# Performance work log

Hardware: AMD Instinct MI355X
Metric: run time of the kernel (lower is better)

The kernel has to match this reference:

```python
import jax, jax.numpy as jnp
import numpy as np

B, T, H, N, D, L, V = 4, 1024, 4, 4096, 256, 6, 256
Dh = N // H  # per-head dim; RoPE max_pos == Dh so T <= Dh
EPS = 1e-5


def _ln(x):
    # LayerNorm over last dim, no affine, eps=1e-5 (torch default)
    m = jnp.mean(x, axis=-1, keepdims=True)
    v = jnp.mean((x - m) ** 2, axis=-1, keepdims=True)
    return (x - m) / jnp.sqrt(v + EPS)


def _rope_tables(seq_len, head_dim):
    inv_freq = 1.0 / (10000.0 ** (jnp.arange(0, head_dim, 2, dtype=jnp.float32) / head_dim))
    t = jnp.arange(seq_len, dtype=jnp.float32)
    freqs = jnp.outer(t, inv_freq)            # [T, Dh/2]
    emb = jnp.concatenate([freqs, freqs], -1)  # [T, Dh]
    return jnp.cos(emb), jnp.sin(emb)


def _rotate_half(x):
    d = x.shape[-1]
    return jnp.concatenate([-x[..., d // 2:], x[..., :d // 2]], axis=-1)


def setup_inputs() -> dict:
    key = jax.random.key(0)
    ks = jax.random.split(key, 6)
    tokens = jax.random.randint(ks[0], (B, T), 0, V)
    emb_w = 0.02 * jax.random.normal(ks[1], (V, D), dtype=jnp.float32)
    E = 0.02 * jax.random.normal(ks[2], (N, D), dtype=jnp.float32)
    Dx = 0.02 * jax.random.normal(ks[3], (H, D, Dh), dtype=jnp.float32)
    Dy = 0.02 * jax.random.normal(ks[4], (H, D, Dh), dtype=jnp.float32)
    readout = 0.02 * jax.random.normal(ks[5], (D, V), dtype=jnp.float32)
    return {"tokens": tokens, "emb_w": emb_w, "E": E, "Dx": Dx, "Dy": Dy, "readout": readout}


def reference(tokens, emb_w, E, Dx, Dy, readout):
    b, t = tokens.shape
    dh = Dx.shape[-1]
    cos, sin = _rope_tables(t, dh)  # [T, Dh], broadcast over B,H
    v = _ln(emb_w[tokens])          # [B, T, D]
    for _ in range(L):
        x = jax.nn.relu(jnp.einsum('btd,hde->bhte', v, Dx))       # [B,H,T,Dh]
        xr = x * cos + _rotate_half(x) * sin                       # RoPE (Q and K share)
        scores = jnp.einsum('bhte,bhse->bhts', xr, xr)             # [B,H,T,T] (no softmax)
        a = jnp.einsum('bhts,bsd->bhtd', scores, v)                # [B,H,T,D]
        y = jax.nn.relu(jnp.einsum('bhtd,hde->bhte', a, Dy)) * x   # [B,H,T,Dh]
        y = jnp.transpose(y, (0, 2, 1, 3)).reshape(b, t, -1)       # [B,T,N]
        v = _ln(v + _ln(y @ E))
    return v @ readout  # [B,T,V]
```

## Files before the change

### kernel.cpp

```cpp
#include <hip/hip_runtime.h>
#include <cstdint>

namespace {

typedef _Float16 f16_t;
typedef _Float16 f16x8 __attribute__((ext_vector_type(8)));
typedef _Float16 f16x4 __attribute__((ext_vector_type(4)));
typedef float    f32x4 __attribute__((ext_vector_type(4)));
typedef float    f32x16 __attribute__((ext_vector_type(16)));

constexpr int Bc = 4, Tc = 1024, Hc = 4, Dc = 256, DHc = 1024, Lc = 6, Vc = 256;
constexpr int HALFc = 512;
constexpr float EPS = 1e-5f;
constexpr long long T4q  = (long long)Tc * 4096;
constexpr long long TDq  = (long long)Tc * Dc;
constexpr long long HDDq = (long long)DHc * Dc;
constexpr long long TBUFq = (long long)Bc * Tc * Dc;

__device__ __forceinline__ int pe_perm(int v) {
  return (v & ~1023) | ((v & 511) << 1) | ((v >> 9) & 1);
}

__device__ __forceinline__ void gload16(const void* g, void* l) {
  __builtin_amdgcn_global_load_lds((const __attribute__((address_space(1))) void*)g,
                                   (__attribute__((address_space(3))) void*)l, 16, 0, 0);
}


template<int NW>
__device__ __forceinline__ void stage_kmaj(const f16_t* __restrict__ P, int k0,
                                           int ld, int c0, f16_t* S, int tid) {
  if constexpr (NW == 16) {
    const int cg = tid & 15;
    const int kp = (tid >> 4) & 31;
    const int jh = (tid >> 9) * 4;
    const int k  = kp * 2;
    const f16x4 r0 = *(const f16x4*)(P + (size_t)(k0 + k) * ld + c0 + cg * 8 + jh);
    const f16x4 r1 = *(const f16x4*)(P + (size_t)(k0 + k + 1) * ld + c0 + cg * 8 + jh);
    #pragma unroll
    for (int j = 0; j < 4; ++j) {
      const int n = cg * 8 + jh + j;
      union { f16_t h[2]; unsigned int u; } pk;
      pk.h[0] = r0[j]; pk.h[1] = r1[j];
      ((unsigned int*)S)[n * 32 + ((((kp >> 2) ^ (n & 7) ^ ((n >> 3) & 7)) & 7) << 2)
                         + (kp & 3)] = pk.u;
    }
  } else {
    const int cg  = tid & 15;
    const int kpb = tid >> 4;
    constexpr int NP = (NW == 4) ? 2 : 1;
    #pragma unroll
    for (int p = 0; p < NP; ++p) {
      const int kp = p * 16 + kpb;
      const int k  = kp * 2;
      const f16x8 r0 = *(const f16x8*)(P + (size_t)(k0 + k) * ld + c0 + cg * 8);
      const f16x8 r1 = *(const f16x8*)(P + (size_t)(k0 + k + 1) * ld + c0 + cg * 8);
      #pragma unroll
      for (int j = 0; j < 8; ++j) {
        const int n = cg * 8 + j;
        union { f16_t h[2]; unsigned int u; } pk;
        pk.h[0] = r0[j]; pk.h[1] = r1[j];
        ((unsigned int*)S)[n * 32 + ((((kp >> 2) ^ (n & 7) ^ ((n >> 3) & 7)) & 7) << 2)
                           + (kp & 3)] = pk.u;
      }
    }
  }
}

template<int EPI, bool AKMAJ, bool BKMAJ, int NW, int KU, bool GRPZ>
__global__ __launch_bounds__(NW * 64)
void gemm_f16(const f16_t* __restrict__ A, long long sAb, long long sAh,
              const f16_t* __restrict__ B, long long sBb, long long sBh,
              void* __restrict__ Cv, long long sCb, long long sCh,
              const f16_t* __restrict__ aux,
              int K, int lda, int ldb, int ldc,
              const float* __restrict__ cosP, const float* __restrict__ sinP)
{
  constexpr int FN2  = (NW == 4) ? 2 : 1;
  constexpr int MT   = (NW == 16) ? 1 : 2;
  constexpr int WCW  = FN2 * 32;
  constexpr int WRH  = MT * 32;
  constexpr int NTHR = NW * 64;
  constexpr int SP   = 1024 / NTHR;
  constexpr int RPP  = NTHR / 8;

  __shared__ __align__(16) f16_t As[KU][128 * 64];
  __shared__ __align__(16) f16_t Bs[KU][128 * 64];

  int bx = blockIdx.x, by = blockIdx.y, bz = blockIdx.z;
  if (GRPZ) {
    const int Xd = gridDim.x, Zd = gridDim.z;
    const int f  = blockIdx.x + Xd * (blockIdx.y + gridDim.y * blockIdx.z);
    bz = f % Zd;
    const int rem = f / Zd;
    bx = rem % Xd;
    by = rem / Xd;
  }

  const int zb = bz >> 2, zh = bz & 3;
  A += zb * sAb + zh * sAh;
  B += zb * sBb + zh * sBh;
  const long long Coff = zb * sCb + zh * sCh;

  const int tid  = threadIdx.x;
  const int lane = tid & 63;
  const int wave = tid >> 6;
  const int wr = (NW == 4) ? (wave >> 1) : (wave >> 2);
  const int wc = (NW == 4) ? (wave & 1)  : (wave & 3);
  const int m0 = by * 128, n0 = bx * 128;

  const int lrow  = tid >> 3;
  const int lslot = tid & 7;

  f32x16 acc[MT][FN2] = {};

  for (int k0 = 0; k0 < K; k0 += KU * 64) {
    #pragma unroll
    for (int u = 0; u < KU; ++u) {
      const int ku = k0 + u * 64;
      if (!AKMAJ) {
        #pragma unroll
        for (int c = 0; c < SP; ++c) {
          const int row  = c * RPP + lrow;
          const int scol = ((lslot ^ (row & 7) ^ ((row >> 3) & 7)) << 3);
          gload16(A + (size_t)(m0 + row) * lda + ku + scol, &As[u][(c * NTHR + tid) * 8]);
        }
      } else {
        stage_kmaj<NW>(A, ku, lda, m0, As[u], tid);
      }
      if (!BKMAJ) {
        #pragma unroll
        for (int c = 0; c < SP; ++c) {
          const int row  = c * RPP + lrow;
          const int scol = ((lslot ^ (row & 7) ^ ((row >> 3) & 7)) << 3);
          gload16(B + (size_t)(n0 + row) * ldb + ku + scol, &Bs[u][(c * NTHR + tid) * 8]);
        }
      } else {
        stage_kmaj<NW>(B, ku, ldb, n0, Bs[u], tid);
      }
    }
    __syncthreads();

    #pragma unroll
    for (int u = 0; u < KU; ++u) {
      #pragma unroll
      for (int kc = 0; kc < 4; ++kc) {
        f16x8 af[MT], bf[FN2];
        #pragma unroll
        for (int m = 0; m < MT; ++m) {
          const int r  = wr * WRH + m * 32 + (lane & 31);
          const int sl = (kc * 2 + (lane >> 5)) ^ (r & 7) ^ ((r >> 3) & 7);
          af[m] = *(const f16x8*)(&As[u][r * 64 + sl * 8]);
        }
        #pragma unroll
        for (int n = 0; n < FN2; ++n) {
          const int r  = wc * WCW + n * 32 + (lane & 31);
          const int sl = (kc * 2 + (lane >> 5)) ^ (r & 7) ^ ((r >> 3) & 7);
          bf[n] = *(const f16x8*)(&Bs[u][r * 64 + sl * 8]);
        }
        #pragma unroll
        for (int m = 0; m < MT; ++m)
          #pragma unroll
          for (int n = 0; n < FN2; ++n)
            acc[m][n] = __builtin_amdgcn_mfma_f32_32x32x16_f16(af[m], bf[n], acc[m][n], 0, 0, 0);
      }
    }
    __syncthreads();
  }

  const int rbase = 4 * (lane >> 5);
  if (EPI == 4) {
    float* C = (float*)Cv + Coff;
    #pragma unroll
    for (int m = 0; m < MT; ++m)
      #pragma unroll
      for (int n = 0; n < FN2; ++n) {
        const int gcol = n0 + wc * WCW + n * 32 + (lane & 31);
        #pragma unroll
        for (int reg = 0; reg < 16; ++reg) {
          const int grow = m0 + wr * WRH + m * 32 + (reg & 3) + 8 * (reg >> 2) + rbase;
          C[(long long)grow * ldc + gcol] = acc[m][n][reg];
        }
      }
  } else if (EPI == 5) {
    f16_t* C = (f16_t*)Cv + Coff;
    #pragma unroll
    for (int m = 0; m < MT; ++m)
      #pragma unroll
      for (int n = 0; n < FN2; ++n) {
        const int gcol = n0 + wc * WCW + n * 32 + (lane & 31);
        const int jj   = (gcol & 1023) >> 1;
        const float sg = (gcol & 1) ? 1.0f : -1.0f;
        #pragma unroll
        for (int reg = 0; reg < 16; ++reg) {
          const int grow = m0 + wr * WRH + m * 32 + (reg & 3) + 8 * (reg >> 2) + rbase;
          const int tt   = grow & (Tc - 1);
          const float val  = fmaxf(acc[m][n][reg], 0.0f);
          const float part = __shfl_xor(val, 1);
          const float c = cosP[tt * HALFc + jj];
          const float s = sinP[tt * HALFc + jj];
          C[(long long)grow * ldc + gcol] = (f16_t)(val * c + part * s * sg);
        }
      }
  } else if (EPI == 2) {
    f16_t* C = (f16_t*)Cv + Coff;
    const f16_t* X = aux + Coff;
    #pragma unroll
    for (int m = 0; m < MT; ++m)
      #pragma unroll
      for (int n = 0; n < FN2; ++n) {
        const int gcol = n0 + wc * WCW + n * 32 + (lane & 31);
        const int jj   = (gcol & 1023) >> 1;
        const float sg = (gcol & 1) ? 1.0f : -1.0f;
        #pragma unroll
        for (int reg = 0; reg < 16; ++reg) {
          const int grow = m0 + wr * WRH + m * 32 + (reg & 3) + 8 * (reg >> 2) + rbase;
          const int tt   = grow & (Tc - 1);
          const long long off = (long long)grow * ldc + gcol;
          const float xrv  = (float)X[off];
          const float part = __shfl_xor(xrv, 1);
          const float c = cosP[tt * HALFc + jj];
          const float s = sinP[tt * HALFc + jj];
          const float xv = xrv * c - part * s * sg;
          C[off] = (f16_t)(fmaxf(acc[m][n][reg], 0.0f) * xv);
        }
      }
  } else {
    f16_t* C = (f16_t*)Cv + Coff;
    #pragma unroll
    for (int m = 0; m < MT; ++m)
      #pragma unroll
      for (int n = 0; n < FN2; ++n) {
        const int gcol = n0 + wc * WCW + n * 32 + (lane & 31);
        #pragma unroll
        for (int reg = 0; reg < 16; ++reg) {
          const int grow = m0 + wr * WRH + m * 32 + (reg & 3) + 8 * (reg >> 2) + rbase;
          C[(long long)grow * ldc + gcol] = (f16_t)acc[m][n][reg];
        }
      }
  }
}

__global__ __launch_bounds__(256)
void transpose_f32_f16(const float* __restrict__ in, f16_t* __restrict__ out,
                       int R, int C, long long sIn, long long sOut,
                       int permR, int permC)
{
  __shared__ float tile[32][33];
  in  += (long long)blockIdx.z * sIn;
  out += (long long)blockIdx.z * sOut;
  const int c0 = blockIdx.x * 32, r0 = blockIdx.y * 32;
  const int tx = threadIdx.x & 31, ty = threadIdx.x >> 5;
  #pragma unroll
  for (int i = 0; i < 32; i += 8)
    tile[ty + i][tx] = in[(long long)(r0 + ty + i) * C + (c0 + tx)];
  __syncthreads();
  #pragma unroll
  for (int i = 0; i < 32; i += 8) {
    int ro = c0 + ty + i;
    int co = r0 + tx;
    if (permR) ro = pe_perm(ro);
    if (permC) co = pe_perm(co);
    out[(long long)ro * R + co] = (f16_t)tile[tx][ty + i];
  }
}

__global__ __launch_bounds__(256)
void init_tables(float* __restrict__ cosT, float* __restrict__ sinT)
{
  const int i = blockIdx.x * 256 + threadIdx.x;
  const int j = i & (HALFc - 1);
  const int t = i >> 9;
  const float inv = expf(-(float)j * (9.210340371976184f / 512.0f));
  const float ang = (float)t * inv;
  cosT[i] = cosf(ang);
  sinT[i] = sinf(ang);
}

__device__ __forceinline__ void block_stats(float val, float* red, float& mean, float& inv_std)
{
  float s1 = val, s2 = val * val;
  #pragma unroll
  for (int o = 1; o < 64; o <<= 1) {
    s1 += __shfl_xor(s1, o);
    s2 += __shfl_xor(s2, o);
  }
  const int lane = threadIdx.x & 63;
  const int w = threadIdx.x >> 6;
  if (lane == 0) { red[w * 2] = s1; red[w * 2 + 1] = s2; }
  __syncthreads();
  s1 = red[0] + red[2] + red[4] + red[6];
  s2 = red[1] + red[3] + red[5] + red[7];
  mean = s1 * (1.0f / Dc);
  const float var = s2 * (1.0f / Dc) - mean * mean;
  inv_std = 1.0f / sqrtf(var + EPS);
  __syncthreads();
}

__global__ __launch_bounds__(256)
void embed_ln(const int* __restrict__ tokens, const float* __restrict__ emb,
              f16_t* __restrict__ v)
{
  __shared__ float red[8];
  const int row = blockIdx.x;
  const int d = threadIdx.x;
  const float val = emb[(long long)tokens[row] * Dc + d];
  float m, is;
  block_stats(val, red, m, is);
  v[(long long)row * Dc + d] = (f16_t)((val - m) * is);
}

__global__ __launch_bounds__(256)
void fuse_ln4(f16_t* __restrict__ v, const f16_t* __restrict__ t)
{
  __shared__ float red[8];
  const long long row = blockIdx.x;
  const int d = threadIdx.x;
  const long long off = row * Dc + d;
  const float tv = (float)t[off] + (float)t[off + TBUFq]
                 + (float)t[off + 2 * TBUFq] + (float)t[off + 3 * TBUFq];
  float m1, is1;
  block_stats(tv, red, m1, is1);
  const float u = (tv - m1) * is1;
  const float wv = (float)v[off] + u;
  float m2, is2;
  block_stats(wv, red, m2, is2);
  v[off] = (f16_t)((wv - m2) * is2);
}

}

extern "C" void kernel_launch(void* const* d_in, const int* in_sizes, int n_in,
                              void* d_out, int out_size, void* d_ws, size_t ws_size,
                              hipStream_t stream)
{
  (void)in_sizes; (void)n_in; (void)out_size; (void)ws_size;
  const int*   tokens  = (const int*)d_in[0];
  const float* emb_w   = (const float*)d_in[1];
  const float* E       = (const float*)d_in[2];
  const float* Dx      = (const float*)d_in[3];
  const float* Dy      = (const float*)d_in[4];
  const float* readout = (const float*)d_in[5];
  float* out = (float*)d_out;

  char* w = (char*)d_ws;
  auto carve = [&](size_t bytes) { char* p = w; w += (bytes + 255) & ~(size_t)255; return p; };
  float* cosT = (float*)carve((size_t)Tc * HALFc * 4);
  float* sinT = (float*)carve((size_t)Tc * HALFc * 4);
  f16_t* v    = (f16_t*)carve((size_t)Bc * Tc * Dc * 2);
  f16_t* xr   = (f16_t*)carve((size_t)Bc * Tc * 4096 * 2);
  f16_t* yb   = (f16_t*)carve((size_t)Bc * Tc * 4096 * 2);
  f16_t* WT   = (f16_t*)carve((size_t)Bc * Dc * 4096 * 2);
  f16_t* a    = (f16_t*)carve((size_t)Bc * Tc * Hc * Dc * 2);
  f16_t* t    = (f16_t*)carve((size_t)4 * TBUFq * 2);
  f16_t* DxT  = (f16_t*)carve((size_t)Hc * DHc * Dc * 2);
  f16_t* DyT  = (f16_t*)carve((size_t)Hc * DHc * Dc * 2);
  f16_t* ET   = (f16_t*)carve((size_t)Dc * Hc * DHc * 2);
  f16_t* RT   = (f16_t*)carve((size_t)Vc * Dc * 2);

  transpose_f32_f16<<<dim3(32, 8, Hc), 256, 0, stream>>>(Dx, DxT, Dc, DHc, HDDq, HDDq, 1, 0);
  transpose_f32_f16<<<dim3(32, 8, Hc), 256, 0, stream>>>(Dy, DyT, Dc, DHc, HDDq, HDDq, 1, 0);
  transpose_f32_f16<<<dim3(8, 128, 1), 256, 0, stream>>>(E, ET, 4096, Dc, 0, 0, 0, 1);
  transpose_f32_f16<<<dim3(8, 8, 1), 256, 0, stream>>>(readout, RT, Dc, Vc, 0, 0, 0, 0);
  init_tables<<<(Tc * HALFc) / 256, 256, 0, stream>>>(cosT, sinT);
  embed_ln<<<Bc * Tc, 256, 0, stream>>>(tokens, emb_w, v);

  for (int l = 0; l < Lc; ++l) {
    gemm_f16<5, false, false, 8, 1, false><<<dim3(32, 32, 1), 512, 0, stream>>>(
        v, 0, 0, DxT, 0, 0, xr, 0, 0, nullptr, Dc, Dc, Dc, 4096, cosT, sinT);
    gemm_f16<0, true, true, 16, 2, true><<<dim3(32, 2, 4), 1024, 0, stream>>>(
        v, 0, TDq, xr, 0, T4q, WT, 0, (long long)Dc * 4096, nullptr,
        Tc, Dc, 4096, 4096, nullptr, nullptr);
    gemm_f16<0, false, false, 16, 2, true><<<dim3(2, 8, 16), 1024, 0, stream>>>(
        xr, T4q, DHc, WT, (long long)Dc * 4096, DHc, a, (long long)Tc * 1024, Dc,
        nullptr, DHc, 4096, 4096, 1024, nullptr, nullptr);
    gemm_f16<2, false, false, 8, 1, true><<<dim3(8, 32, 4), 512, 0, stream>>>(
        a, 0, Dc, DyT, 0, HDDq, yb, 0, DHc, xr, Dc, 1024, Dc, 4096, cosT, sinT);
    gemm_f16<0, false, false, 16, 2, true><<<dim3(2, 32, 4), 1024, 0, stream>>>(
        yb, 0, DHc, ET, 0, DHc, t, 0, TBUFq, nullptr, DHc, 4096, 4096, Dc,
        nullptr, nullptr);
    fuse_ln4<<<Bc * Tc, 256, 0, stream>>>(v, t);
  }

  gemm_f16<4, false, false, 16, 2, false><<<dim3(2, 32, 1), 1024, 0, stream>>>(
      v, 0, 0, RT, 0, 0, out, 0, 0, nullptr, Dc, Dc, Dc, Vc, nullptr, nullptr);
}
```

Measured before the change: 694.3 us.

## Fuse Dy GEMM, RoPE-gated epilogue, and E projection into one kernel

Replaces the separate Dy GEMM (writing the y buffer) and the E GEMM with a single kernel. Each block computes a 128-column slice of y in registers, applies relu and multiplies by the recovered x, stages the result in shared memory, and immediately multiplies by the matching E slice. Partial sums are split into 8 buffers along the head dimension and reduced in the layer-norm kernel. This removes the round trip of the 32MB y tensor through global memory, at the cost of a non-pipelined, synchronous load loop, only 256 blocks, and more partial-sum traffic.

```diff
diff --git a/kernel.cpp b/kernel.cpp
--- a/kernel.cpp
+++ b/kernel.cpp
@@ -202,29 +202,6 @@
           C[(long long)grow * ldc + gcol] = (f16_t)(val * c + part * s * sg);
         }
       }
-  } else if (EPI == 2) {
-    f16_t* C = (f16_t*)Cv + Coff;
-    const f16_t* X = aux + Coff;
-    #pragma unroll
-    for (int m = 0; m < MT; ++m)
-      #pragma unroll
-      for (int n = 0; n < FN2; ++n) {
-        const int gcol = n0 + wc * WCW + n * 32 + (lane & 31);
-        const int jj   = (gcol & 1023) >> 1;
-        const float sg = (gcol & 1) ? 1.0f : -1.0f;
-        #pragma unroll
-        for (int reg = 0; reg < 16; ++reg) {
-          const int grow = m0 + wr * WRH + m * 32 + (reg & 3) + 8 * (reg >> 2) + rbase;
-          const int tt   = grow & (Tc - 1);
-          const long long off = (long long)grow * ldc + gcol;
-          const float xrv  = (float)X[off];
-          const float part = __shfl_xor(xrv, 1);
-          const float c = cosP[tt * HALFc + jj];
-          const float s = sinP[tt * HALFc + jj];
-          const float xv = xrv * c - part * s * sg;
-          C[off] = (f16_t)(fmaxf(acc[m][n][reg], 0.0f) * xv);
-        }
-      }
   } else {
     f16_t* C = (f16_t*)Cv + Coff;
     #pragma unroll
@@ -238,6 +215,117 @@
           C[(long long)grow * ldc + gcol] = (f16_t)acc[m][n][reg];
         }
       }
+  }
+}
+
+__global__ __launch_bounds__(1024)
+void gemm56(const f16_t* __restrict__ a,
+            const f16_t* __restrict__ DyT,
+            const f16_t* __restrict__ xr,
+            const f16_t* __restrict__ ET,
+            f16_t* __restrict__ t,
+            const float* __restrict__ cosP, const float* __restrict__ sinP)
+{
+  __shared__ __align__(16) f16_t As1[128 * 64];
+  __shared__ __align__(16) f16_t Bs1[128 * 64];
+  __shared__ __align__(16) f16_t As2[2][128 * 64];
+  __shared__ __align__(16) f16_t Bs2[2][128 * 64];
+
+  const int f  = blockIdx.x + 32 * blockIdx.z;
+  const int bz = f & 7;
+  const int bx = f >> 3;
+  const int h = bz >> 1, half = bz & 1;
+  const int m0 = bx * 128;
+
+  const int tid  = threadIdx.x;
+  const int lane = tid & 63;
+  const int wave = tid >> 6;
+  const int wr = wave >> 2, wc = wave & 3;
+  const int lrow  = tid >> 3;
+  const int lslot = tid & 7;
+  const int rbase = 4 * (lane >> 5);
+
+  f32x16 tacc[2] = {};
+
+  for (int hb = 0; hb < 4; ++hb) {
+    const int he0 = h * 1024 + half * 512 + hb * 128;
+
+    f32x16 yacc = {};
+    for (int k0 = 0; k0 < 256; k0 += 64) {
+      const int scol = ((lslot ^ (lrow & 7) ^ ((lrow >> 3) & 7)) << 3);
+      gload16(a + (size_t)(m0 + lrow) * 1024 + h * 256 + k0 + scol, &As1[tid * 8]);
+      gload16(DyT + (size_t)(he0 + lrow) * 256 + k0 + scol, &Bs1[tid * 8]);
+      __syncthreads();
+      #pragma unroll
+      for (int kc = 0; kc < 4; ++kc) {
+        const int rA  = wr * 32 + (lane & 31);
+        const int slA = (kc * 2 + (lane >> 5)) ^ (rA & 7) ^ ((rA >> 3) & 7);
+        const f16x8 af = *(const f16x8*)(&As1[rA * 64 + slA * 8]);
+        const int rB  = wc * 32 + (lane & 31);
+        const int slB = (kc * 2 + (lane >> 5)) ^ (rB & 7) ^ ((rB >> 3) & 7);
+        const f16x8 bf = *(const f16x8*)(&Bs1[rB * 64 + slB * 8]);
+        yacc = __builtin_amdgcn_mfma_f32_32x32x16_f16(af, bf, yacc, 0, 0, 0);
+      }
+      __syncthreads();
+    }
+
+    {
+      const int heL  = wc * 32 + (lane & 31);
+      const int gcol = he0 + heL;
+      const int jj   = (gcol & 1023) >> 1;
+      const float sg = (gcol & 1) ? 1.0f : -1.0f;
+      const int kk   = heL & 63;
+      const int buf  = heL >> 6;
+      #pragma unroll
+      for (int reg = 0; reg < 16; ++reg) {
+        const int rowL = wr * 32 + (reg & 3) + 8 * (reg >> 2) + rbase;
+        const int grow = m0 + rowL;
+        const int tt   = grow & (Tc - 1);
+        const float xrv  = (float)xr[(size_t)grow * 4096 + gcol];
+        const float part = __shfl_xor(xrv, 1);
+        const float c = cosP[tt * HALFc + jj];
+        const float s = sinP[tt * HALFc + jj];
+        const float xv = xrv * c - part * s * sg;
+        const float yv = fmaxf(yacc[reg], 0.0f) * xv;
+        const int sl = (kk >> 3) ^ (rowL & 7) ^ ((rowL >> 3) & 7);
+        As2[buf][rowL * 64 + sl * 8 + (kk & 7)] = (f16_t)yv;
+      }
+    }
+    __syncthreads();
+
+    #pragma unroll
+    for (int ks2 = 0; ks2 < 2; ++ks2) {
+      const int scol = ((lslot ^ (lrow & 7) ^ ((lrow >> 3) & 7)) << 3);
+      gload16(ET + (size_t)lrow * 4096 + he0 + ks2 * 64 + scol, &Bs2[0][tid * 8]);
+      gload16(ET + (size_t)(128 + lrow) * 4096 + he0 + ks2 * 64 + scol, &Bs2[1][tid * 8]);
+      __syncthreads();
+      #pragma unroll
+      for (int kc = 0; kc < 4; ++kc) {
+        const int rA  = wr * 32 + (lane & 31);
+        const int slA = (kc * 2 + (lane >> 5)) ^ (rA & 7) ^ ((rA >> 3) & 7);
+        const f16x8 af = *(const f16x8*)(&As2[ks2][rA * 64 + slA * 8]);
+        #pragma unroll
+        for (int n = 0; n < 2; ++n) {
+          const int d    = wc * 64 + n * 32 + (lane & 31);
+          const int rloc = d & 127;
+          const int sl   = (kc * 2 + (lane >> 5)) ^ (rloc & 7) ^ ((rloc >> 3) & 7);
+          const f16x8 bf = *(const f16x8*)(&Bs2[d >> 7][rloc * 64 + sl * 8]);
+          tacc[n] = __builtin_amdgcn_mfma_f32_32x32x16_f16(af, bf, tacc[n], 0, 0, 0);
+        }
+      }
+      __syncthreads();
+    }
+  }
+
+  f16_t* T = t + (long long)bz * TBUFq;
+  #pragma unroll
+  for (int n = 0; n < 2; ++n) {
+    const int gcol = wc * 64 + n * 32 + (lane & 31);
+    #pragma unroll
+    for (int reg = 0; reg < 16; ++reg) {
+      const int grow = m0 + wr * 32 + (reg & 3) + 8 * (reg >> 2) + rbase;
+      T[(size_t)grow * 256 + gcol] = (f16_t)tacc[n][reg];
+    }
   }
 }
 
@@ -311,14 +399,15 @@
 }
 
 __global__ __launch_bounds__(256)
-void fuse_ln4(f16_t* __restrict__ v, const f16_t* __restrict__ t)
+void fuse_ln8(f16_t* __restrict__ v, const f16_t* __restrict__ t)
 {
   __shared__ float red[8];
   const long long row = blockIdx.x;
   const int d = threadIdx.x;
   const long long off = row * Dc + d;
-  const float tv = (float)t[off] + (float)t[off + TBUFq]
-                 + (float)t[off + 2 * TBUFq] + (float)t[off + 3 * TBUFq];
+  float tv = 0.0f;
+  #pragma unroll
+  for (int s = 0; s < 8; ++s) tv += (float)t[off + s * TBUFq];
   float m1, is1;
   block_stats(tv, red, m1, is1);
   const float u = (tv - m1) * is1;
@@ -349,10 +438,9 @@
   float* sinT = (float*)carve((size_t)Tc * HALFc * 4);
   f16_t* v    = (f16_t*)carve((size_t)Bc * Tc * Dc * 2);
   f16_t* xr   = (f16_t*)carve((size_t)Bc * Tc * 4096 * 2);
-  f16_t* yb   = (f16_t*)carve((size_t)Bc * Tc * 4096 * 2);
   f16_t* WT   = (f16_t*)carve((size_t)Bc * Dc * 4096 * 2);
   f16_t* a    = (f16_t*)carve((size_t)Bc * Tc * Hc * Dc * 2);
-  f16_t* t    = (f16_t*)carve((size_t)4 * TBUFq * 2);
+  f16_t* t    = (f16_t*)carve((size_t)8 * TBUFq * 2);
   f16_t* DxT  = (f16_t*)carve((size_t)Hc * DHc * Dc * 2);
   f16_t* DyT  = (f16_t*)carve((size_t)Hc * DHc * Dc * 2);
   f16_t* ET   = (f16_t*)carve((size_t)Dc * Hc * DHc * 2);
@@ -374,12 +462,8 @@
     gemm_f16<0, false, false, 16, 2, true><<<dim3(2, 8, 16), 1024, 0, stream>>>(
         xr, T4q, DHc, WT, (long long)Dc * 4096, DHc, a, (long long)Tc * 1024, Dc,
         nullptr, DHc, 4096, 4096, 1024, nullptr, nullptr);
-    gemm_f16<2, false, false, 8, 1, true><<<dim3(8, 32, 4), 512, 0, stream>>>(
-        a, 0, Dc, DyT, 0, HDDq, yb, 0, DHc, xr, Dc, 1024, Dc, 4096, cosT, sinT);
-    gemm_f16<0, false, false, 16, 2, true><<<dim3(2, 32, 4), 1024, 0, stream>>>(
-        yb, 0, DHc, ET, 0, DHc, t, 0, TBUFq, nullptr, DHc, 4096, 4096, Dc,
-        nullptr, nullptr);
-    fuse_ln4<<<Bc * Tc, 256, 0, stream>>>(v, t);
+    gemm56<<<dim3(32, 1, 8), 1024, 0, stream>>>(a, DyT, xr, ET, t, cosT, sinT);
+    fuse_ln8<<<Bc * Tc, 256, 0, stream>>>(v, t);
   }
 
   gemm_f16<4, false, false, 16, 2, false><<<dim3(2, 32, 1), 1024, 0, stream>>>(
```

Result: slower. 811.9 us (+16.9%).
